# Kernel tuning notes

Hardware: AMD Instinct MI355X
Metric: run time of the kernel (lower is better)

The kernel has to match this reference:

```python
import jax, jax.numpy as jnp
import numpy as np

B, N, M = 64, 4096, 128


def setup_inputs() -> dict:
    key = jax.random.key(0)
    x = jax.random.normal(key, (B, N, M), dtype=jnp.float32)
    return {"x": x}


def reference(x):
    # Original loops over channels M, applying a 1D FFT along the N axis to
    # each (batch, N) slice. Equivalent batched form: FFT along axis=1.
    f = jnp.fft.fft(x.astype(jnp.complex64), axis=1)  # (B, N, M) complex64
    return (jnp.real(f), jnp.imag(f))
```

## Files before the change

### kernel.cpp

```cpp
#include <hip/hip_runtime.h>
#include <hip/hip_fp16.h>

#define B 64
#define N 4096
#define M 128

constexpr int T   = 256;
constexpr int NWG = 1024;

__device__ __forceinline__ float2 cadd(float2 a, float2 b){ return make_float2(a.x+b.x, a.y+b.y); }
__device__ __forceinline__ float2 csub(float2 a, float2 b){ return make_float2(a.x-b.x, a.y-b.y); }
__device__ __forceinline__ float2 cmul(float2 a, float2 b){ return make_float2(a.x*b.x - a.y*b.y, a.x*b.y + a.y*b.x); }
__device__ __forceinline__ float2 mulnegi(float2 a){ return make_float2(a.y, -a.x); }
__device__ __forceinline__ float2 muli(float2 a)  { return make_float2(-a.y, a.x); }
__device__ __forceinline__ float2 cis(float ang){ float s, c; __sincosf(ang, &s, &c); return make_float2(c, s); }
__device__ __forceinline__ float2 h2f(__half2 h){ return __half22float2(h); }
__device__ __forceinline__ __half2 f2h(float2 v){ return __floats2half2_rn(v.x, v.y); }

__device__ __constant__ const float W64R[8] = {
    1.0f, 0.995184726672197f, 0.980785280403230f, 0.956940335732209f,
    0.923879532511287f, 0.881921264348355f, 0.831469612302545f, 0.773010453362737f };
__device__ __constant__ const float W64I[8] = {
    0.0f, -0.098017140329561f, -0.195090322016128f, -0.290284677254462f,
    -0.382683432365090f, -0.471396736825998f, -0.555570233019602f, -0.634393284163645f };

__device__ __forceinline__ void dft8(float2 t[8]) {
    float2 e0=cadd(t[0],t[4]), e1=csub(t[0],t[4]);
    float2 e2=cadd(t[2],t[6]), e3=csub(t[2],t[6]);
    float2 E0=cadd(e0,e2), E2=csub(e0,e2);
    float2 E1=cadd(e1,mulnegi(e3)), E3=cadd(e1,muli(e3));
    float2 o0=cadd(t[1],t[5]), o1=csub(t[1],t[5]);
    float2 o2=cadd(t[3],t[7]), o3=csub(t[3],t[7]);
    float2 O0=cadd(o0,o2), O2=csub(o0,o2);
    float2 O1=cadd(o1,mulnegi(o3)), O3=cadd(o1,muli(o3));
    const float C = 0.70710678118654752f;
    float2 w1O1 = make_float2(C*(O1.x+O1.y), C*(O1.y-O1.x));
    float2 w2O2 = mulnegi(O2);
    float2 w3O3 = make_float2(C*(O3.y-O3.x), -C*(O3.x+O3.y));
    t[0]=cadd(E0,O0);   t[4]=csub(E0,O0);
    t[1]=cadd(E1,w1O1); t[5]=csub(E1,w1O1);
    t[2]=cadd(E2,w2O2); t[6]=csub(E2,w2O2);
    t[3]=cadd(E3,w3O3); t[7]=csub(E3,w3O3);
}

__device__ __forceinline__ int lslot(int k1, int n2, int mc) {
    return (k1 << 8) | ((n2 ^ (k1 & 7)) << 2) | mc;
}

__global__ __launch_bounds__(T, 2)
void fft_one(const float* __restrict__ x, float* __restrict__ out) {
    extern __shared__ __half2 lz[];

    const int bid = blockIdx.x;
    const int b   = ((bid >> 7) << 3) | (bid & 7);
    const int mcg = (bid >> 3) & 15;
    const int tid = threadIdx.x;
    const int mc  = tid & 3;
    const int rp  = tid >> 2;

    const float* xb = x + (size_t)b * N * M + mcg * 8 + mc * 2;

    __half2 pk[8][8];

    #pragma unroll
    for (int bb = 0; bb < 8; ++bb) {
        float2 t[8];
        #pragma unroll
        for (int a = 0; a < 8; ++a)
            t[a] = *(const float2*)(xb + (size_t)(64*(8*a+bb) + rp) * M);
        dft8(t);
        #pragma unroll
        for (int d = 0; d < 8; ++d) pk[bb][d] = f2h(t[d]);
    }
    {
        const float2 ws = cis(-6.2831853071795864f * (float)rp / 4096.0f);
        const float2 w8 = cis(-6.2831853071795864f * (float)rp / 512.0f);
        float2 pd = make_float2(1.f, 0.f);
        #pragma unroll
        for (int d = 0; d < 8; ++d) {
            const float2 wd = make_float2(W64R[d], W64I[d]);
            float2 t[8];
            t[0] = h2f(pk[0][d]);
            float2 w = wd;
            #pragma unroll
            for (int bb = 1; bb < 8; ++bb) {
                t[bb] = cmul(h2f(pk[bb][d]), w);
                w = cmul(w, wd);
            }
            dft8(t);
            float2 ac = pd;
            #pragma unroll
            for (int c = 0; c < 8; ++c) {
                lz[lslot(8*c+d, rp, mc)] = f2h(cmul(t[c], ac));
                ac = cmul(ac, w8);
            }
            pd = cmul(pd, ws);
        }
    }
    __syncthreads();

    #pragma unroll
    for (int bb = 0; bb < 8; ++bb) {
        float2 t[8];
        #pragma unroll
        for (int a = 0; a < 8; ++a)
            t[a] = h2f(lz[lslot(rp, 8*a+bb, mc)]);
        dft8(t);
        #pragma unroll
        for (int d = 0; d < 8; ++d) pk[bb][d] = f2h(t[d]);
    }
    #pragma unroll
    for (int d = 0; d < 8; ++d) {
        const float2 wd = make_float2(W64R[d], W64I[d]);
        float2 t[8];
        t[0] = h2f(pk[0][d]);
        float2 w = wd;
        #pragma unroll
        for (int bb = 1; bb < 8; ++bb) {
            t[bb] = cmul(h2f(pk[bb][d]), w);
            w = cmul(w, wd);
        }
        dft8(t);
        #pragma unroll
        for (int c = 0; c < 8; ++c)
            lz[lslot(rp, 8*c+d, mc)] = f2h(t[c]);
    }
    __syncthreads();

    float* outRe = out + (size_t)b * N * M + mcg * 8 + mc * 2;
    float* outIm = outRe + (size_t)B * N * M;
    const int r = rp;
    #pragma unroll 4
    for (int j = 0; j < 64; ++j) {
        int k   = (j << 6) | r;
        int kk  = (N - k) & (N - 1);
        int k1p = kk & 63, k2p = kk >> 6;
        float2 Zk = h2f(lz[lslot(r,   j,   mc)]);
        float2 Zm = h2f(lz[lslot(k1p, k2p, mc)]);
        float2 re = make_float2(0.5f * (Zk.x + Zm.x), 0.5f * (Zk.y + Zm.y));
        float2 im = make_float2(0.5f * (Zk.y - Zm.y), 0.5f * (Zm.x - Zk.x));
        *(float2*)(outRe + (size_t)k * M) = re;
        *(float2*)(outIm + (size_t)k * M) = im;
    }
}

extern "C" void kernel_launch(void* const* d_in, const int* in_sizes, int n_in,
                              void* d_out, int out_size, void* d_ws, size_t ws_size,
                              hipStream_t stream) {
    const float* x = (const float*)d_in[0];
    float* out = (float*)d_out;
    const int lds_bytes = 64 * 64 * 4 * (int)sizeof(__half2);
    hipFuncSetAttribute((const void*)fft_one,
                        hipFuncAttributeMaxDynamicSharedMemorySize, lds_bytes);
    fft_one<<<NWG, T, lds_bytes, stream>>>(x, out);
}
```

Baseline: 147.7 us.

## Split each FFT column across two threads with wave shuffles to double occupancy

The block doubles to 512 threads, and each column's 64-point radix-8x8 sub-FFT is now split between two threads (s=0/1). Partial results are exchanged through a warp-lane xor-4 shuffle, which halves per-thread registers (pk 8x8 to 4x8) and raises launch bounds to 4 blocks per SM. The aim is to increase latency hiding for the global loads and stores and the LDS traffic. In exchange it adds shuffle traffic and select logic, and 2.5 blocks' worth of LDS per CU may limit how much residency actually increases.

```diff
diff --git a/kernel.cpp b/kernel.cpp
--- a/kernel.cpp
+++ b/kernel.cpp
@@ -5,7 +5,7 @@
 #define N 4096
 #define M 128
 
-constexpr int T   = 256;
+constexpr int T   = 512;
 constexpr int NWG = 1024;
 
 __device__ __forceinline__ float2 cadd(float2 a, float2 b){ return make_float2(a.x+b.x, a.y+b.y); }
@@ -16,6 +16,11 @@
 __device__ __forceinline__ float2 cis(float ang){ float s, c; __sincosf(ang, &s, &c); return make_float2(c, s); }
 __device__ __forceinline__ float2 h2f(__half2 h){ return __half22float2(h); }
 __device__ __forceinline__ __half2 f2h(float2 v){ return __floats2half2_rn(v.x, v.y); }
+__device__ __forceinline__ __half2 shxor4(__half2 v) {
+    unsigned u = *(unsigned*)&v;
+    unsigned r = (unsigned)__shfl_xor((int)u, 4, 64);
+    return *(__half2*)&r;
+}
 
 __device__ __constant__ const float W64R[8] = {
     1.0f, 0.995184726672197f, 0.980785280403230f, 0.956940335732209f,
@@ -47,7 +52,7 @@
     return (k1 << 8) | ((n2 ^ (k1 & 7)) << 2) | mc;
 }
 
-__global__ __launch_bounds__(T, 2)
+__global__ __launch_bounds__(T, 4)
 void fft_one(const float* __restrict__ x, float* __restrict__ out) {
     extern __shared__ __half2 lz[];
 
@@ -56,42 +61,62 @@
     const int mcg = (bid >> 3) & 15;
     const int tid = threadIdx.x;
     const int mc  = tid & 3;
-    const int rp  = tid >> 2;
+    const int s   = (tid >> 2) & 1;
+    const int rp  = tid >> 3;
 
     const float* xb = x + (size_t)b * N * M + mcg * 8 + mc * 2;
 
-    __half2 pk[8][8];
+    __half2 pk[4][8];
+    __half2 rcv[4][4];
 
     #pragma unroll
-    for (int bb = 0; bb < 8; ++bb) {
+    for (int cc = 0; cc < 4; ++cc) {
+        const int bb = 4 * s + cc;
         float2 t[8];
         #pragma unroll
         for (int a = 0; a < 8; ++a)
-            t[a] = *(const float2*)(xb + (size_t)(64*(8*a+bb) + rp) * M);
+            t[a] = *(const float2*)(xb + (size_t)(64 * (8 * a + bb) + rp) * M);
         dft8(t);
         #pragma unroll
-        for (int d = 0; d < 8; ++d) pk[bb][d] = f2h(t[d]);
+        for (int d = 0; d < 8; ++d) pk[cc][d] = f2h(t[d]);
     }
+    #pragma unroll
+    for (int cc = 0; cc < 4; ++cc)
+        #pragma unroll
+        for (int dd = 0; dd < 4; ++dd) {
+            __half2 lo = pk[cc][dd], hi = pk[cc][4 + dd];
+            rcv[cc][dd] = shxor4(s ? lo : hi);
+        }
     {
-        const float2 ws = cis(-6.2831853071795864f * (float)rp / 4096.0f);
-        const float2 w8 = cis(-6.2831853071795864f * (float)rp / 512.0f);
-        float2 pd = make_float2(1.f, 0.f);
+        const float ang = -6.2831853071795864f * (float)rp;
+        const float2 ws  = cis(ang / 4096.0f);
+        const float2 ws4 = cis(ang / 1024.0f);
+        const float2 w8  = cis(ang / 512.0f);
+        float2 pd = s ? ws4 : make_float2(1.f, 0.f);
         #pragma unroll
-        for (int d = 0; d < 8; ++d) {
-            const float2 wd = make_float2(W64R[d], W64I[d]);
+        for (int dd = 0; dd < 4; ++dd) {
+            float2 w1a = make_float2(W64R[dd],     W64I[dd]);
+            float2 w1b = make_float2(W64R[4 + dd], W64I[4 + dd]);
+            float2 w1 = s ? w1b : w1a;
             float2 t[8];
-            t[0] = h2f(pk[0][d]);
-            float2 w = wd;
             #pragma unroll
-            for (int bb = 1; bb < 8; ++bb) {
-                t[bb] = cmul(h2f(pk[bb][d]), w);
-                w = cmul(w, wd);
+            for (int cc = 0; cc < 4; ++cc) {
+                float2 own = h2f(s ? pk[cc][4 + dd] : pk[cc][dd]);
+                float2 rv  = h2f(rcv[cc][dd]);
+                t[cc]     = s ? rv  : own;
+                t[4 + cc] = s ? own : rv;
+            }
+            {
+                float2 w = w1;
+                #pragma unroll
+                for (int bb = 1; bb < 8; ++bb) { t[bb] = cmul(t[bb], w); w = cmul(w, w1); }
             }
             dft8(t);
+            const int dp = 4 * s + dd;
             float2 ac = pd;
             #pragma unroll
             for (int c = 0; c < 8; ++c) {
-                lz[lslot(8*c+d, rp, mc)] = f2h(cmul(t[c], ac));
+                lz[lslot(8 * c + dp, rp, mc)] = f2h(cmul(t[c], ac));
                 ac = cmul(ac, w8);
             }
             pd = cmul(pd, ws);
@@ -100,42 +125,58 @@
     __syncthreads();
 
     #pragma unroll
-    for (int bb = 0; bb < 8; ++bb) {
+    for (int cc = 0; cc < 4; ++cc) {
+        const int bb = 4 * s + cc;
         float2 t[8];
         #pragma unroll
         for (int a = 0; a < 8; ++a)
-            t[a] = h2f(lz[lslot(rp, 8*a+bb, mc)]);
+            t[a] = h2f(lz[lslot(rp, 8 * a + bb, mc)]);
         dft8(t);
         #pragma unroll
-        for (int d = 0; d < 8; ++d) pk[bb][d] = f2h(t[d]);
+        for (int d = 0; d < 8; ++d) pk[cc][d] = f2h(t[d]);
     }
     #pragma unroll
-    for (int d = 0; d < 8; ++d) {
-        const float2 wd = make_float2(W64R[d], W64I[d]);
+    for (int cc = 0; cc < 4; ++cc)
+        #pragma unroll
+        for (int dd = 0; dd < 4; ++dd) {
+            __half2 lo = pk[cc][dd], hi = pk[cc][4 + dd];
+            rcv[cc][dd] = shxor4(s ? lo : hi);
+        }
+    #pragma unroll
+    for (int dd = 0; dd < 4; ++dd) {
+        float2 w1a = make_float2(W64R[dd],     W64I[dd]);
+        float2 w1b = make_float2(W64R[4 + dd], W64I[4 + dd]);
+        float2 w1 = s ? w1b : w1a;
         float2 t[8];
-        t[0] = h2f(pk[0][d]);
-        float2 w = wd;
         #pragma unroll
-        for (int bb = 1; bb < 8; ++bb) {
-            t[bb] = cmul(h2f(pk[bb][d]), w);
-            w = cmul(w, wd);
+        for (int cc = 0; cc < 4; ++cc) {
+            float2 own = h2f(s ? pk[cc][4 + dd] : pk[cc][dd]);
+            float2 rv  = h2f(rcv[cc][dd]);
+            t[cc]     = s ? rv  : own;
+            t[4 + cc] = s ? own : rv;
+        }
+        {
+            float2 w = w1;
+            #pragma unroll
+            for (int bb = 1; bb < 8; ++bb) { t[bb] = cmul(t[bb], w); w = cmul(w, w1); }
         }
         dft8(t);
+        const int dp = 4 * s + dd;
         #pragma unroll
         for (int c = 0; c < 8; ++c)
-            lz[lslot(rp, 8*c+d, mc)] = f2h(t[c]);
+            lz[lslot(rp, 8 * c + dp, mc)] = f2h(t[c]);
     }
     __syncthreads();
 
     float* outRe = out + (size_t)b * N * M + mcg * 8 + mc * 2;
     float* outIm = outRe + (size_t)B * N * M;
-    const int r = rp;
     #pragma unroll 4
-    for (int j = 0; j < 64; ++j) {
-        int k   = (j << 6) | r;
-        int kk  = (N - k) & (N - 1);
+    for (int jj = 0; jj < 32; ++jj) {
+        int j  = 32 * s + jj;
+        int k  = (j << 6) | rp;
+        int kk = (N - k) & (N - 1);
         int k1p = kk & 63, k2p = kk >> 6;
-        float2 Zk = h2f(lz[lslot(r,   j,   mc)]);
+        float2 Zk = h2f(lz[lslot(rp,  j,   mc)]);
         float2 Zm = h2f(lz[lslot(k1p, k2p, mc)]);
         float2 re = make_float2(0.5f * (Zk.x + Zm.x), 0.5f * (Zk.y + Zm.y));
         float2 im = make_float2(0.5f * (Zk.y - Zm.y), 0.5f * (Zm.x - Zk.x));
```

Result: slower. 232.2 us (+57.2%).
